# Optimization experiments

Measured on AMD Instinct MI355X. Metric: run time of the kernel, lower is better.

Reference implementation:

```python
import jax, jax.numpy as jnp
import numpy as np

B, P, C = 8, 8192, 91            # images, proposals/image, classes (incl. background)
PRE_NMS_TOPK = 1000              # fixed-size candidate set per image for NMS
DET_PER_IMG = 100                # detections_per_img
SCORE_THRESH = 0.05
NMS_THRESH = 0.5
MIN_SIZE = 0.01                  # remove_small_boxes min_size
BBOX_W = (10.0, 10.0, 5.0, 5.0)  # bbox_reg_weights
BBOX_XFORM_CLIP = float(np.log(1000.0 / 16.0))
NEG = -1e9


def setup_inputs() -> dict:
    key = jax.random.key(0)
    k1, k2, k3, k4, k5, k6 = jax.random.split(key, 6)
    H, W = 800, 1333
    class_logits = jax.random.normal(k1, (B, P, C), jnp.float32)
    box_regression = jax.random.normal(k2, (B, P, 4 * C), jnp.float32) * 0.5
    # random valid proposal boxes inside the image
    cx = jax.random.uniform(k3, (B, P)) * W
    cy = jax.random.uniform(k4, (B, P)) * H
    bw = jax.random.uniform(k5, (B, P)) * 200.0 + 16.0
    bh = jax.random.uniform(k6, (B, P)) * 200.0 + 16.0
    x1 = jnp.clip(cx - 0.5 * bw, 0.0, W - 1.0)
    y1 = jnp.clip(cy - 0.5 * bh, 0.0, H - 1.0)
    x2 = jnp.clip(cx + 0.5 * bw, x1 + 1.0, float(W))
    y2 = jnp.clip(cy + 0.5 * bh, y1 + 1.0, float(H))
    proposals = jnp.stack([x1, y1, x2, y2], axis=-1)
    image_hw = jnp.array([H, W], jnp.int32)
    return {"class_logits": class_logits, "box_regression": box_regression,
            "proposals": proposals, "image_hw": image_hw}


def _iou_matrix(b):
    # b: [K,4] -> [K,K] pairwise IoU
    area = (b[:, 2] - b[:, 0]) * (b[:, 3] - b[:, 1])
    lt = jnp.maximum(b[:, None, :2], b[None, :, :2])
    rb = jnp.minimum(b[:, None, 2:], b[None, :, 2:])
    wh = jnp.clip(rb - lt, 0.0)
    inter = wh[..., 0] * wh[..., 1]
    return inter / (area[:, None] + area[None, :] - inter + 1e-9)


def _postprocess(class_logits, box_regression, proposals, image_hw):
    Hf = image_hw[0].astype(jnp.float32)
    Wf = image_hw[1].astype(jnp.float32)
    wx, wy, ww, wh = BBOX_W
    # --- BoxCoder.decode ---
    widths = proposals[..., 2] - proposals[..., 0]            # [B,P]
    heights = proposals[..., 3] - proposals[..., 1]
    ctr_x = proposals[..., 0] + 0.5 * widths
    ctr_y = proposals[..., 1] + 0.5 * heights
    rel = box_regression.reshape(B, P, C, 4)
    dx = rel[..., 0] / wx
    dy = rel[..., 1] / wy
    dw = jnp.minimum(rel[..., 2] / ww, BBOX_XFORM_CLIP)
    dh = jnp.minimum(rel[..., 3] / wh, BBOX_XFORM_CLIP)
    pcx = dx * widths[..., None] + ctr_x[..., None]           # [B,P,C]
    pcy = dy * heights[..., None] + ctr_y[..., None]
    pw = jnp.exp(dw) * widths[..., None]
    ph = jnp.exp(dh) * heights[..., None]
    # --- clip_boxes_to_image ---
    x1 = jnp.clip(pcx - 0.5 * pw, 0.0, Wf)
    y1 = jnp.clip(pcy - 0.5 * ph, 0.0, Hf)
    x2 = jnp.clip(pcx + 0.5 * pw, 0.0, Wf)
    y2 = jnp.clip(pcy + 0.5 * ph, 0.0, Hf)
    boxes = jnp.stack([x1, y1, x2, y2], axis=-1)              # [B,P,C,4]
    scores = jax.nn.softmax(class_logits, axis=-1)            # [B,P,C]
    # drop background class 0, flatten (proposal, class) candidates
    M = P * (C - 1)
    boxes_f = boxes[:, :, 1:, :].reshape(B, M, 4)
    scores_f = scores[:, :, 1:].reshape(B, M)
    labels_f = jnp.broadcast_to(jnp.tile(jnp.arange(1, C, dtype=jnp.int32), P), (B, M))
    # score threshold + remove_small_boxes as score masking (fixed shapes)
    ws = boxes_f[..., 2] - boxes_f[..., 0]
    hs = boxes_f[..., 3] - boxes_f[..., 1]
    valid = (scores_f > SCORE_THRESH) & (ws >= MIN_SIZE) & (hs >= MIN_SIZE)
    mscores = jnp.where(valid, scores_f, NEG)
    offset_scale = jnp.maximum(Hf, Wf) + 1.0

    def per_image(b, s, l):
        # pre-NMS top-k candidates (sorted descending, matching NMS score order)
        sk, idx = jax.lax.top_k(s, PRE_NMS_TOPK)              # [K]
        bk = b[idx]                                           # [K,4]
        lk = l[idx]
        valid_k = sk > NEG / 2
        # batched_nms via per-class coordinate offsets
        bo = bk + (lk.astype(jnp.float32) * offset_scale)[:, None]
        iou = _iou_matrix(bo)                                 # [K,K]
        K = PRE_NMS_TOPK
        rng = jnp.arange(K)
        def body(i, supp):
            active = jnp.logical_and(jnp.logical_not(supp[i]), valid_k[i])
            new = active & (iou[i] > NMS_THRESH) & (rng > i)
            return supp | new
        supp = jax.lax.fori_loop(0, K, body, jnp.zeros((K,), bool))
        keep = jnp.logical_and(jnp.logical_not(supp), valid_k)
        fs = jnp.where(keep, sk, NEG)
        fsd, fidx = jax.lax.top_k(fs, DET_PER_IMG)
        fb = bk[fidx]
        fl = lk[fidx]
        ok = fsd > NEG / 2
        return (jnp.where(ok[:, None], fb, 0.0),
                jnp.where(ok, fsd, 0.0),
                jnp.where(ok, fl, 0))

    return jax.vmap(per_image)(boxes_f, mscores, labels_f)


def reference(class_logits, box_regression, proposals, image_hw):
    boxes, scores, labels = _postprocess(class_logits, box_regression, proposals, image_hw)
    return boxes, scores, labels  # [B,100,4] float, [B,100] float, [B,100] int32
```

## Files before the change

kernel.cpp:

```cpp
#include <hip/hip_runtime.h>

namespace {

constexpr int NB = 8, NP = 8192, NC = 91;
constexpr int KTOP = 1000, NDET = 100;
constexpr int MROWS = 1024;
constexpr int NBUCK = 4096, SORTN = 4096;
constexpr int NLAB = 90;
constexpr int BPI = 512;
constexpr int BCAP = 304;
constexpr float SCORE_T = 0.05f;
constexpr float MIN_SZ = 0.01f;
constexpr float NMS_T = 0.5f;
constexpr float CLIPV = 4.135166556742356f;
constexpr float NEGV = -1e9f;

typedef unsigned long long ull;

__device__ __forceinline__ void decode_box(const float4& pr, const float4& rel,
                                           float Wf, float Hf,
                                           float& x1, float& y1, float& x2, float& y2) {
  float w = pr.z - pr.x, h = pr.w - pr.y;
  float cx = pr.x + 0.5f * w, cy = pr.y + 0.5f * h;
  float dx = rel.x / 10.0f, dy = rel.y / 10.0f;
  float dw = fminf(rel.z / 5.0f, CLIPV), dh = fminf(rel.w / 5.0f, CLIPV);
  float pcx = dx * w + cx, pcy = dy * h + cy;
  float pw = expf(dw) * w, ph = expf(dh) * h;
  x1 = fminf(fmaxf(pcx - 0.5f * pw, 0.0f), Wf);
  y1 = fminf(fmaxf(pcy - 0.5f * ph, 0.0f), Hf);
  x2 = fminf(fmaxf(pcx + 0.5f * pw, 0.0f), Wf);
  y2 = fminf(fmaxf(pcy + 0.5f * ph, 0.0f), Hf);
}

__device__ __forceinline__ int score_bucket(unsigned bits) {
  return min((int)((bits - 0x3D000000u) >> 14), NBUCK - 1);
}

__global__ __launch_bounds__(256) void k_candidates(
    const float* __restrict__ logits, const float* __restrict__ boxreg,
    const float* __restrict__ props, const int* __restrict__ hw,
    ull* __restrict__ dense, int* __restrict__ bcnt) {
  __shared__ float sh[16 * NC];
  __shared__ ull stage[16][20];
  __shared__ int gcnt[16];
  __shared__ int gbase[16];
  int tid = threadIdx.x;
  int base = blockIdx.x * 16;
  const float4* src4 = reinterpret_cast<const float4*>(logits + (size_t)base * NC);
  float4* sh4 = reinterpret_cast<float4*>(sh);
  for (int i = tid; i < (16 * NC) / 4; i += 256) sh4[i] = src4[i];
  __syncthreads();

  int lane = tid & 63;
  int l16 = lane & 15;
  int grp = lane >> 4;
  int wv = tid >> 6;
  int lp = wv * 4 + grp;
  int gw = base + lp;
  int p = gw & (NP - 1);
  float Hf = (float)hw[0], Wf = (float)hw[1];
  const float* row = sh + lp * NC;

  float zreg[6];
  float m = -3.0e38f;
#pragma unroll
  for (int k = 0; k < 6; ++k) {
    int c = k * 16 + l16;
    float z = (c < NC) ? row[c] : -3.0e38f;
    zreg[k] = z;
    m = fmaxf(m, z);
  }
#pragma unroll
  for (int d = 1; d < 16; d <<= 1) m = fmaxf(m, __shfl_xor(m, d, 64));
  float S = 0.0f;
#pragma unroll
  for (int k = 0; k < 6; ++k) {
    int c = k * 16 + l16;
    S += (c < NC) ? expf(zreg[k] - m) : 0.0f;
  }
#pragma unroll
  for (int d = 1; d < 16; d <<= 1) S += __shfl_xor(S, d, 64);

  float invS = 1.0f / S;
  float thr = m + logf(SCORE_T * S) - 1e-3f;

  float4 pr = reinterpret_cast<const float4*>(props)[gw];
  const float4* relrow = reinterpret_cast<const float4*>(boxreg + (size_t)gw * 4 * NC);
  unsigned below = (1u << l16) - 1u;
  int n = 0;
#pragma unroll
  for (int k = 0; k < 6; ++k) {
    int c = k * 16 + l16;
    bool ok = (c >= 1) && (c < NC) && (zreg[k] > thr);
    float sc = 0.0f;
    if (ok) {
      sc = expf(zreg[k] - m) * invS;
      ok = sc > SCORE_T;
      if (ok) {
        float4 rel = relrow[c];
        float x1, y1, x2, y2;
        decode_box(pr, rel, Wf, Hf, x1, y1, x2, y2);
        ok = ((x2 - x1) >= MIN_SZ) && ((y2 - y1) >= MIN_SZ);
      }
    }
    ull bal = __ballot(ok);
    unsigned gm = (unsigned)((bal >> (grp * 16)) & 0xFFFFull);
    if (ok) {
      int pos = n + __popc(gm & below);
      unsigned bits = __float_as_uint(sc);
      int idx = p * (NC - 1) + (c - 1);
      if (pos < 20) stage[lp][pos] = ((ull)bits << 32) | (unsigned)(~(unsigned)idx);
    }
    n += __popc(gm);
  }
  if (l16 == 0) gcnt[lp] = min(n, 20);
  __syncthreads();
  if (tid == 0) {
    int off[16];
    int tot = 0;
#pragma unroll
    for (int g = 0; g < 16; ++g) { off[g] = tot; tot += gcnt[g]; }
#pragma unroll
    for (int g = 0; g < 16; ++g) gbase[g] = off[g];
    bcnt[blockIdx.x] = tot;
  }
  __syncthreads();
  ull* dst = dense + (size_t)blockIdx.x * BCAP;
  for (int j = l16; j < gcnt[lp]; j += 16) dst[gbase[lp] + j] = stage[lp][j];
}

__global__ __launch_bounds__(1024) void k_select(
    const ull* __restrict__ dense, const int* __restrict__ bcnt,
    const float* __restrict__ boxreg, const float* __restrict__ props,
    const int* __restrict__ hw,
    float* __restrict__ topk_score, float* __restrict__ det_box,
    int* __restrict__ det_label, int* __restrict__ keep, int* __restrict__ nvalid) {
  __shared__ int h[NBUCK];
  __shared__ int cur[NBUCK];
  __shared__ ull sk[SORTN];
  __shared__ int sbs;
  int b = blockIdx.x, tid = threadIdx.x;
#pragma unroll
  for (int k = 0; k < NBUCK / 1024; ++k) h[tid + k * 1024] = 0;
  if (tid == 0) sbs = 0;
  __syncthreads();
  int seg = tid >> 1;
  int par = tid & 1;
  int gseg = b * BPI + seg;
  int scnt = bcnt[gseg];
  const ull* sptr = dense + (size_t)gseg * BCAP;
  for (int j = par; j < scnt; j += 2)
    atomicAdd(&h[score_bucket((unsigned)(sptr[j] >> 32))], 1);
  __syncthreads();
  for (int d = 1; d < NBUCK; d <<= 1) {
    int v[NBUCK / 1024];
#pragma unroll
    for (int k = 0; k < NBUCK / 1024; ++k) {
      int i = tid + k * 1024;
      v[k] = h[i] + ((i + d < NBUCK) ? h[i + d] : 0);
    }
    __syncthreads();
#pragma unroll
    for (int k = 0; k < NBUCK / 1024; ++k) h[tid + k * 1024] = v[k];
    __syncthreads();
  }
#pragma unroll
  for (int k = 0; k < NBUCK / 1024; ++k) {
    int i = tid + k * 1024;
    if (h[i] >= KTOP && (i == NBUCK - 1 || h[i + 1] < KTOP)) sbs = i;
  }
  __syncthreads();
#pragma unroll
  for (int k = 0; k < NBUCK / 1024; ++k) {
    int i = tid + k * 1024;
    cur[i] = (i + 1 < NBUCK) ? h[i + 1] : 0;
  }
  __syncthreads();
  int sb = sbs;
  int total = min(h[sb], SORTN);
  for (int j = par; j < scnt; j += 2) {
    ull key = sptr[j];
    int bk = score_bucket((unsigned)(key >> 32));
    if (bk < sb) continue;
    int pos = atomicAdd(&cur[bk], 1);
    if (pos < SORTN) sk[pos] = key;
  }
  __syncthreads();
  float Hf = (float)hw[0], Wf = (float)hw[1];
  for (int i = tid; i < total; i += 1024) {
    ull key = sk[i];
    int bk = score_bucket((unsigned)(key >> 32));
    int s0 = (bk + 1 < NBUCK) ? h[bk + 1] : 0;
    int e = min(cur[bk], total);
    int r = s0;
    for (int j = s0; j < e; ++j) r += (sk[j] > key) ? 1 : 0;
    if (r < KTOP) {
      int og = b * KTOP + r;
      topk_score[og] = __uint_as_float((unsigned)(key >> 32));
      int fidx = (int)(~(unsigned)key);
      int p = fidx / (NC - 1), c = fidx % (NC - 1) + 1;
      float4 pr = reinterpret_cast<const float4*>(props)[b * NP + p];
      float4 rel =
          reinterpret_cast<const float4*>(boxreg + (size_t)(b * NP + p) * 4 * NC)[c];
      float x1, y1, x2, y2;
      decode_box(pr, rel, Wf, Hf, x1, y1, x2, y2);
      det_box[(size_t)og * 4 + 0] = x1;
      det_box[(size_t)og * 4 + 1] = y1;
      det_box[(size_t)og * 4 + 2] = x2;
      det_box[(size_t)og * 4 + 3] = y2;
      det_label[og] = c;
      keep[og] = 1;
    }
  }
  int valid_n = min(total, KTOP);
  for (int r = valid_n + tid; r < KTOP; r += 1024) {
    int og = b * KTOP + r;
    topk_score[og] = NEGV;
    det_box[(size_t)og * 4 + 0] = 0.0f;
    det_box[(size_t)og * 4 + 1] = 0.0f;
    det_box[(size_t)og * 4 + 2] = 0.0f;
    det_box[(size_t)og * 4 + 3] = 0.0f;
    det_label[og] = 0;
    keep[og] = 0;
  }
  if (tid == 0) nvalid[b] = valid_n;
}

__global__ __launch_bounds__(64) void k_nms(
    const int* __restrict__ nvalid, const float* __restrict__ det_box,
    const int* __restrict__ det_label, int* __restrict__ keep) {
  __shared__ int list[MROWS];
  __shared__ float4 mbx[64];
  __shared__ unsigned char sup[MROWS];
  int bb = blockIdx.x;
  int b = bb / NLAB;
  int lab = bb % NLAB + 1;
  int lane = threadIdx.x;
  int nv = nvalid[b];
  ull below = (1ull << lane) - 1ull;
  const int* ll = det_label + b * KTOP;
  int c = 0;
  for (int base = 0; base < KTOP; base += 64) {
    int i = base + lane;
    bool mb = (i < KTOP) && (i < nv) && (ll[i] == lab);
    ull bal = __ballot(mb);
    if (mb) list[c + __popcll(bal & below)] = i;
    c += __popcll(bal);
  }
  if (c <= 1) return;
  __syncthreads();
  const float4* bbx = reinterpret_cast<const float4*>(det_box) + (size_t)b * KTOP;
  if (c <= 64) {
    if (lane < c) mbx[lane] = bbx[list[lane]];
    __syncthreads();
    float4 bx = mbx[(lane < c) ? lane : 0];
    float area = (bx.z - bx.x) * (bx.w - bx.y);
    ull col = 0ull;
    for (int i = 0; i + 1 < c; ++i) {
      float4 bi = mbx[i];
      float ai = (bi.z - bi.x) * (bi.w - bi.y);
      float ltx = fmaxf(bi.x, bx.x), lty = fmaxf(bi.y, bx.y);
      float rbx = fminf(bi.z, bx.z), rby = fminf(bi.w, bx.w);
      float iw = fmaxf(rbx - ltx, 0.0f), ih = fmaxf(rby - lty, 0.0f);
      float inter = iw * ih;
      float iou = inter / (ai + area - inter + 1e-9f);
      if ((lane > i) && (lane < c) && (iou > NMS_T)) col |= (1ull << i);
    }
    if (__ballot(col != 0ull)) {
      unsigned s = 0u;
      for (int i = 0; i + 1 < c; ++i) {
        ull act = __ballot(s == 0u);
        s |= (unsigned)((act >> i) & (col >> i) & 1ull);
      }
      if (lane < c && s) keep[b * KTOP + list[lane]] = 0;
    }
  } else {
    if (lane == 0) {
      for (int a = 0; a < c; ++a) sup[a] = 0;
      for (int a = 0; a < c; ++a) {
        if (sup[a]) continue;
        float4 bi = bbx[list[a]];
        float ai = (bi.z - bi.x) * (bi.w - bi.y);
        for (int e = a + 1; e < c; ++e) {
          if (sup[e]) continue;
          float4 bj = bbx[list[e]];
          float aj = (bj.z - bj.x) * (bj.w - bj.y);
          float ltx = fmaxf(bi.x, bj.x), lty = fmaxf(bi.y, bj.y);
          float rbx = fminf(bi.z, bj.z), rby = fminf(bi.w, bj.w);
          float iw = fmaxf(rbx - ltx, 0.0f), ih = fmaxf(rby - lty, 0.0f);
          float inter = iw * ih;
          if (inter / (ai + aj - inter + 1e-9f) > NMS_T) sup[e] = 1;
        }
      }
      for (int a = 0; a < c; ++a)
        if (sup[a]) keep[b * KTOP + list[a]] = 0;
    }
  }
}

__global__ __launch_bounds__(256) void k_output(
    const float* __restrict__ topk_score, const float* __restrict__ det_box,
    const int* __restrict__ det_label, const int* __restrict__ keep,
    float* __restrict__ out) {
  __shared__ int kp[MROWS];
  __shared__ int pf[MROWS];
  int b = blockIdx.x, tid = threadIdx.x;
  for (int i = tid; i < MROWS; i += 256) {
    int v = (i < KTOP) ? keep[b * KTOP + i] : 0;
    kp[i] = v;
    pf[i] = v;
  }
  __syncthreads();
  for (int d = 1; d < MROWS; d <<= 1) {
    int v[4];
#pragma unroll
    for (int k = 0; k < 4; ++k) {
      int i = tid + k * 256;
      v[k] = pf[i] + ((i >= d) ? pf[i - d] : 0);
    }
    __syncthreads();
#pragma unroll
    for (int k = 0; k < 4; ++k) pf[tid + k * 256] = v[k];
    __syncthreads();
  }
  int total = min(pf[KTOP - 1], NDET);
  float* ob = out;
  float* os = out + (size_t)NB * NDET * 4;
  float* ol = os + (size_t)NB * NDET;
  for (int i = tid; i < KTOP; i += 256) {
    if (kp[i]) {
      int r = pf[i] - 1;
      if (r < NDET) {
        ob[((size_t)b * NDET + r) * 4 + 0] = det_box[((size_t)b * KTOP + i) * 4 + 0];
        ob[((size_t)b * NDET + r) * 4 + 1] = det_box[((size_t)b * KTOP + i) * 4 + 1];
        ob[((size_t)b * NDET + r) * 4 + 2] = det_box[((size_t)b * KTOP + i) * 4 + 2];
        ob[((size_t)b * NDET + r) * 4 + 3] = det_box[((size_t)b * KTOP + i) * 4 + 3];
        os[b * NDET + r] = topk_score[b * KTOP + i];
        ol[b * NDET + r] = (float)det_label[b * KTOP + i];
      }
    }
  }
  for (int r = total + tid; r < NDET; r += 256) {
    ob[((size_t)b * NDET + r) * 4 + 0] = 0.0f;
    ob[((size_t)b * NDET + r) * 4 + 1] = 0.0f;
    ob[((size_t)b * NDET + r) * 4 + 2] = 0.0f;
    ob[((size_t)b * NDET + r) * 4 + 3] = 0.0f;
    os[b * NDET + r] = 0.0f;
    ol[b * NDET + r] = 0.0f;
  }
}

}

extern "C" void kernel_launch(void* const* d_in, const int* in_sizes, int n_in,
                              void* d_out, int out_size, void* d_ws, size_t ws_size,
                              hipStream_t stream) {
  const float* logits = (const float*)d_in[0];
  const float* boxreg = (const float*)d_in[1];
  const float* props = (const float*)d_in[2];
  const int* hw = (const int*)d_in[3];

  char* ws = (char*)d_ws;
  size_t off = 0;
  auto alloc = [&](size_t bytes) -> void* {
    void* p = ws + off;
    off += (bytes + 255) & ~(size_t)255;
    return p;
  };
  ull* dense = (ull*)alloc((size_t)NB * BPI * BCAP * 8);
  int* bcnt = (int*)alloc((size_t)NB * BPI * 4);
  float* topk_score = (float*)alloc((size_t)NB * KTOP * 4);
  float* det_box = (float*)alloc((size_t)NB * KTOP * 16);
  int* det_label = (int*)alloc((size_t)NB * KTOP * 4);
  int* keep = (int*)alloc((size_t)NB * KTOP * 4);
  int* nvalid = (int*)alloc(NB * 4);

  k_candidates<<<(NB * NP) / 16, 256, 0, stream>>>(logits, boxreg, props, hw,
                                                   dense, bcnt);
  k_select<<<NB, 1024, 0, stream>>>(dense, bcnt, boxreg, props, hw,
                                    topk_score, det_box, det_label, keep, nvalid);
  k_nms<<<NB * NLAB, 64, 0, stream>>>(nvalid, det_box, det_label, keep);
  k_output<<<NB, 256, 0, stream>>>(topk_score, det_box, det_label, keep, (float*)d_out);
}
```

Before: 62.48 us.

## Fuse select, per-class NMS and output compaction into one per-image kernel

New measurement: 74.29 us. 18.9% more time.

```diff
diff --git a/kernel.cpp b/kernel.cpp
--- a/kernel.cpp
+++ b/kernel.cpp
@@ -4,7 +4,6 @@
 
 constexpr int NB = 8, NP = 8192, NC = 91;
 constexpr int KTOP = 1000, NDET = 100;
-constexpr int MROWS = 1024;
 constexpr int NBUCK = 4096, SORTN = 4096;
 constexpr int NLAB = 90;
 constexpr int BPI = 512;
@@ -129,16 +128,17 @@
   for (int j = l16; j < gcnt[lp]; j += 16) dst[gbase[lp] + j] = stage[lp][j];
 }
 
-__global__ __launch_bounds__(1024) void k_select(
+__global__ __launch_bounds__(1024) void k_fused(
     const ull* __restrict__ dense, const int* __restrict__ bcnt,
     const float* __restrict__ boxreg, const float* __restrict__ props,
     const int* __restrict__ hw,
     float* __restrict__ topk_score, float* __restrict__ det_box,
-    int* __restrict__ det_label, int* __restrict__ keep, int* __restrict__ nvalid) {
-  __shared__ int h[NBUCK];
-  __shared__ int cur[NBUCK];
-  __shared__ ull sk[SORTN];
+    int* __restrict__ det_label, float* __restrict__ out) {
+  __shared__ __align__(16) char smem[65536];
   __shared__ int sbs;
+  int* h = (int*)smem;
+  int* cur = (int*)(smem + 16384);
+  ull* sk = (ull*)(smem + 32768);
   int b = blockIdx.x, tid = threadIdx.x;
 #pragma unroll
   for (int k = 0; k < NBUCK / 1024; ++k) h[tid + k * 1024] = 0;
@@ -209,7 +209,6 @@
       det_box[(size_t)og * 4 + 2] = x2;
       det_box[(size_t)og * 4 + 3] = y2;
       det_label[og] = c;
-      keep[og] = 1;
     }
   }
   int valid_n = min(total, KTOP);
@@ -221,126 +220,117 @@
     det_box[(size_t)og * 4 + 2] = 0.0f;
     det_box[(size_t)og * 4 + 3] = 0.0f;
     det_label[og] = 0;
-    keep[og] = 0;
-  }
-  if (tid == 0) nvalid[b] = valid_n;
-}
-
-__global__ __launch_bounds__(64) void k_nms(
-    const int* __restrict__ nvalid, const float* __restrict__ det_box,
-    const int* __restrict__ det_label, int* __restrict__ keep) {
-  __shared__ int list[MROWS];
-  __shared__ float4 mbx[64];
-  __shared__ unsigned char sup[MROWS];
-  int bb = blockIdx.x;
-  int b = bb / NLAB;
-  int lab = bb % NLAB + 1;
-  int lane = threadIdx.x;
-  int nv = nvalid[b];
+  }
+  __syncthreads();
+
+  float4* boxes = (float4*)smem;
+  int* labels = (int*)(smem + 16384);
+  int* keepsh = (int*)(smem + 20480);
+  int* wlist = (int*)(smem + 24576);
+  int* pf = (int*)(smem + 28672);
+  {
+    const float4* gb = reinterpret_cast<const float4*>(det_box) + (size_t)b * KTOP;
+    const int* gl = det_label + b * KTOP;
+    for (int k = 0; k < 2; ++k) {
+      int i = tid + k * 1024;
+      if (i < 1024) {
+        if (i < KTOP) {
+          boxes[i] = gb[i];
+          labels[i] = gl[i];
+        } else {
+          boxes[i] = make_float4(0.f, 0.f, 0.f, 0.f);
+          labels[i] = 0;
+        }
+        keepsh[i] = (i < valid_n) ? 1 : 0;
+      }
+    }
+  }
+  __syncthreads();
+  int wv = tid >> 6, lane = tid & 63;
   ull below = (1ull << lane) - 1ull;
-  const int* ll = det_label + b * KTOP;
-  int c = 0;
-  for (int base = 0; base < KTOP; base += 64) {
-    int i = base + lane;
-    bool mb = (i < KTOP) && (i < nv) && (ll[i] == lab);
-    ull bal = __ballot(mb);
-    if (mb) list[c + __popcll(bal & below)] = i;
-    c += __popcll(bal);
-  }
-  if (c <= 1) return;
-  __syncthreads();
-  const float4* bbx = reinterpret_cast<const float4*>(det_box) + (size_t)b * KTOP;
-  if (c <= 64) {
-    if (lane < c) mbx[lane] = bbx[list[lane]];
-    __syncthreads();
-    float4 bx = mbx[(lane < c) ? lane : 0];
-    float area = (bx.z - bx.x) * (bx.w - bx.y);
-    ull col = 0ull;
-    for (int i = 0; i + 1 < c; ++i) {
-      float4 bi = mbx[i];
-      float ai = (bi.z - bi.x) * (bi.w - bi.y);
-      float ltx = fmaxf(bi.x, bx.x), lty = fmaxf(bi.y, bx.y);
-      float rbx = fminf(bi.z, bx.z), rby = fminf(bi.w, bx.w);
-      float iw = fmaxf(rbx - ltx, 0.0f), ih = fmaxf(rby - lty, 0.0f);
-      float inter = iw * ih;
-      float iou = inter / (ai + area - inter + 1e-9f);
-      if ((lane > i) && (lane < c) && (iou > NMS_T)) col |= (1ull << i);
-    }
-    if (__ballot(col != 0ull)) {
-      unsigned s = 0u;
+  for (int L = wv; L < NLAB; L += 16) {
+    int lab = L + 1;
+    int* list = wlist + wv * 64;
+    int c = 0;
+#pragma unroll
+    for (int base = 0; base < 1024; base += 64) {
+      int i = base + lane;
+      bool mb = (i < valid_n) && (labels[i] == lab);
+      ull bal = __ballot(mb);
+      if (mb) {
+        int pos = c + __popcll(bal & below);
+        if (pos < 64) list[pos] = i;
+      }
+      c += __popcll(bal);
+    }
+    if (c <= 1) continue;
+    if (c <= 64) {
+      float4 bx = boxes[list[(lane < c) ? lane : 0]];
+      float area = (bx.z - bx.x) * (bx.w - bx.y);
+      ull col = 0ull;
       for (int i = 0; i + 1 < c; ++i) {
-        ull act = __ballot(s == 0u);
-        s |= (unsigned)((act >> i) & (col >> i) & 1ull);
-      }
-      if (lane < c && s) keep[b * KTOP + list[lane]] = 0;
-    }
-  } else {
-    if (lane == 0) {
-      for (int a = 0; a < c; ++a) sup[a] = 0;
-      for (int a = 0; a < c; ++a) {
-        if (sup[a]) continue;
-        float4 bi = bbx[list[a]];
+        float4 bi = boxes[list[i]];
         float ai = (bi.z - bi.x) * (bi.w - bi.y);
-        for (int e = a + 1; e < c; ++e) {
-          if (sup[e]) continue;
-          float4 bj = bbx[list[e]];
+        float ltx = fmaxf(bi.x, bx.x), lty = fmaxf(bi.y, bx.y);
+        float rbx = fminf(bi.z, bx.z), rby = fminf(bi.w, bx.w);
+        float iw = fmaxf(rbx - ltx, 0.0f), ih = fmaxf(rby - lty, 0.0f);
+        float inter = iw * ih;
+        float iou = inter / (ai + area - inter + 1e-9f);
+        if ((lane > i) && (lane < c) && (iou > NMS_T)) col |= (1ull << i);
+      }
+      if (__ballot(col != 0ull)) {
+        unsigned s = 0u;
+        for (int i = 0; i + 1 < c; ++i) {
+          ull act = __ballot(s == 0u);
+          s |= (unsigned)((act >> i) & (col >> i) & 1ull);
+        }
+        if (lane < c && s) keepsh[list[lane]] = 0;
+      }
+    } else if (lane == 0) {
+      for (int i = 0; i < valid_n; ++i) {
+        if (labels[i] != lab || !keepsh[i]) continue;
+        float4 bi = boxes[i];
+        float ai = (bi.z - bi.x) * (bi.w - bi.y);
+        for (int j = i + 1; j < valid_n; ++j) {
+          if (labels[j] != lab || !keepsh[j]) continue;
+          float4 bj = boxes[j];
           float aj = (bj.z - bj.x) * (bj.w - bj.y);
           float ltx = fmaxf(bi.x, bj.x), lty = fmaxf(bi.y, bj.y);
           float rbx = fminf(bi.z, bj.z), rby = fminf(bi.w, bj.w);
           float iw = fmaxf(rbx - ltx, 0.0f), ih = fmaxf(rby - lty, 0.0f);
           float inter = iw * ih;
-          if (inter / (ai + aj - inter + 1e-9f) > NMS_T) sup[e] = 1;
+          if (inter / (ai + aj - inter + 1e-9f) > NMS_T) keepsh[j] = 0;
         }
       }
-      for (int a = 0; a < c; ++a)
-        if (sup[a]) keep[b * KTOP + list[a]] = 0;
-    }
-  }
-}
-
-__global__ __launch_bounds__(256) void k_output(
-    const float* __restrict__ topk_score, const float* __restrict__ det_box,
-    const int* __restrict__ det_label, const int* __restrict__ keep,
-    float* __restrict__ out) {
-  __shared__ int kp[MROWS];
-  __shared__ int pf[MROWS];
-  int b = blockIdx.x, tid = threadIdx.x;
-  for (int i = tid; i < MROWS; i += 256) {
-    int v = (i < KTOP) ? keep[b * KTOP + i] : 0;
-    kp[i] = v;
-    pf[i] = v;
-  }
-  __syncthreads();
-  for (int d = 1; d < MROWS; d <<= 1) {
-    int v[4];
-#pragma unroll
-    for (int k = 0; k < 4; ++k) {
-      int i = tid + k * 256;
-      v[k] = pf[i] + ((i >= d) ? pf[i - d] : 0);
-    }
+    }
+  }
+  __syncthreads();
+
+  pf[tid] = keepsh[tid];
+  __syncthreads();
+  for (int d = 1; d < 1024; d <<= 1) {
+    int v = pf[tid] + ((tid >= d) ? pf[tid - d] : 0);
     __syncthreads();
-#pragma unroll
-    for (int k = 0; k < 4; ++k) pf[tid + k * 256] = v[k];
+    pf[tid] = v;
     __syncthreads();
   }
-  int total = min(pf[KTOP - 1], NDET);
+  int total_k = min(pf[KTOP - 1], NDET);
   float* ob = out;
   float* os = out + (size_t)NB * NDET * 4;
   float* ol = os + (size_t)NB * NDET;
-  for (int i = tid; i < KTOP; i += 256) {
-    if (kp[i]) {
-      int r = pf[i] - 1;
-      if (r < NDET) {
-        ob[((size_t)b * NDET + r) * 4 + 0] = det_box[((size_t)b * KTOP + i) * 4 + 0];
-        ob[((size_t)b * NDET + r) * 4 + 1] = det_box[((size_t)b * KTOP + i) * 4 + 1];
-        ob[((size_t)b * NDET + r) * 4 + 2] = det_box[((size_t)b * KTOP + i) * 4 + 2];
-        ob[((size_t)b * NDET + r) * 4 + 3] = det_box[((size_t)b * KTOP + i) * 4 + 3];
-        os[b * NDET + r] = topk_score[b * KTOP + i];
-        ol[b * NDET + r] = (float)det_label[b * KTOP + i];
-      }
-    }
-  }
-  for (int r = total + tid; r < NDET; r += 256) {
+  if (tid < KTOP && keepsh[tid]) {
+    int r = pf[tid] - 1;
+    if (r < NDET) {
+      float4 bx = boxes[tid];
+      ob[((size_t)b * NDET + r) * 4 + 0] = bx.x;
+      ob[((size_t)b * NDET + r) * 4 + 1] = bx.y;
+      ob[((size_t)b * NDET + r) * 4 + 2] = bx.z;
+      ob[((size_t)b * NDET + r) * 4 + 3] = bx.w;
+      os[b * NDET + r] = topk_score[b * KTOP + tid];
+      ol[b * NDET + r] = (float)labels[tid];
+    }
+  }
+  for (int r = total_k + tid; r < NDET; r += 1024) {
     ob[((size_t)b * NDET + r) * 4 + 0] = 0.0f;
     ob[((size_t)b * NDET + r) * 4 + 1] = 0.0f;
     ob[((size_t)b * NDET + r) * 4 + 2] = 0.0f;
@@ -372,13 +362,9 @@
   float* topk_score = (float*)alloc((size_t)NB * KTOP * 4);
   float* det_box = (float*)alloc((size_t)NB * KTOP * 16);
   int* det_label = (int*)alloc((size_t)NB * KTOP * 4);
-  int* keep = (int*)alloc((size_t)NB * KTOP * 4);
-  int* nvalid = (int*)alloc(NB * 4);
 
   k_candidates<<<(NB * NP) / 16, 256, 0, stream>>>(logits, boxreg, props, hw,
                                                    dense, bcnt);
-  k_select<<<NB, 1024, 0, stream>>>(dense, bcnt, boxreg, props, hw,
-                                    topk_score, det_box, det_label, keep, nvalid);
-  k_nms<<<NB * NLAB, 64, 0, stream>>>(nvalid, det_box, det_label, keep);
-  k_output<<<NB, 256, 0, stream>>>(topk_score, det_box, det_label, keep, (float*)d_out);
-}
+  k_fused<<<NB, 1024, 0, stream>>>(dense, bcnt, boxreg, props, hw,
+                                   topk_score, det_box, det_label, (float*)d_out);
+}
```
